# Kernel optimization log

Hardware: AMD Instinct MI355X
Metric: run time of the kernel (lower is better)

## Reference

```python
import jax, jax.numpy as jnp
import numpy as np

SR, WINLEN, HOPLEN = 44100.0, 1024.0, 256.0
B, C, T = 32, 384, 512
MAX_DUR = 0.1          # setup caps duration at 0.1s -> max 13 frames/token
MAX_FRAMES = T * 13    # static padded frame length (jit-compatible upper bound)


def setup_inputs() -> dict:
    key = jax.random.key(0)
    k1, k2, k3, k4 = jax.random.split(key, 4)
    x = jax.random.normal(k1, (B, C, T), dtype=jnp.float32)
    # integer-valued note pitches stored as float (module detaches them anyway)
    notepitch = jax.random.randint(k2, (B, T), 0, 80).astype(jnp.float32)
    duration = jax.random.uniform(k3, (B, T), dtype=jnp.float32) * MAX_DUR
    x_lengths = jax.random.randint(k4, (B,), 1, T + 1)
    return {"x": x, "notepitch": notepitch, "duration": duration, "x_lengths": x_lengths}


def _repeat_counts(duration):
    # expand_size rule from the module:
    #   sr*d - winlen > 0 -> max((sr*d - winlen)/hoplen, 1)
    #   d == 0            -> 0
    #   else              -> 1
    # then int() truncation, clamped at 0.
    fr = SR * duration
    r = jnp.where(fr - WINLEN > 0.0,
                  jnp.maximum((fr - WINLEN) / HOPLEN, 1.0),
                  jnp.where(duration == 0.0, 0.0, 1.0))
    return r.astype(jnp.int32)  # trunc toward zero (values are >= 0)


def reference(x, notepitch, duration, x_lengths):
    r = _repeat_counts(duration)                 # [B, T]
    cum = jnp.cumsum(r, axis=1)                  # [B, T]
    frame_lengths = cum[:, -1]                   # [B]
    pos = jnp.arange(MAX_FRAMES)                 # [F]
    # token index producing each output frame: repeat-interleave via searchsorted
    tok = jax.vmap(lambda c: jnp.searchsorted(c, pos, side="right"))(cum)  # [B, F]
    tok = jnp.minimum(tok, x.shape[-1] - 1)
    mask = pos[None, :] < frame_lengths[:, None]  # [B, F]
    xt = jnp.transpose(x, (0, 2, 1))              # [B, T, C]
    expanded = jnp.take_along_axis(xt, tok[:, :, None], axis=1)  # [B, F, C]
    out = jnp.where(mask[:, :, None], expanded, 0.0)
    out = jnp.transpose(out, (0, 2, 1))           # [B, C, F]
    pitch = jnp.take_along_axis(notepitch, tok, axis=1)
    # module round-trips pitch through LongTensor -> truncation to int
    pitch = jnp.where(mask, pitch.astype(jnp.int32).astype(jnp.float32), 0.0)
    return out, pitch, frame_lengths.astype(jnp.int32)
```

## Files before the change

kernel.cpp:

```cpp
#include <hip/hip_runtime.h>

#define BB 32
#define CC 384
#define TT 512
#define MAXF 6656
#define CG 8
#define NCHUNK 7

typedef float f32x4 __attribute__((ext_vector_type(4)));

__device__ __forceinline__ void nt_store4(float* p, float a, float b, float c, float d) {
    f32x4 v; v.x = a; v.y = b; v.z = c; v.w = d;
    __builtin_nontemporal_store(v, (f32x4*)p);
}

__device__ __forceinline__ void nt_zero4(float* p) {
    f32x4 v = (f32x4)0.0f;
    __builtin_nontemporal_store(v, (f32x4*)p);
}

__device__ __forceinline__ int rep_count(float d) {
    float fr = 44100.0f * d;
    float rf;
    if (fr - 1024.0f > 0.0f) rf = fmaxf((fr - 1024.0f) * (1.0f / 256.0f), 1.0f);
    else rf = (d == 0.0f) ? 0.0f : 1.0f;
    return (int)rf;
}

__global__ __launch_bounds__(256) void lr_fused_co_kernel(
        const float* __restrict__ x,
        const float* __restrict__ notepitch,
        const float* __restrict__ duration,
        float* __restrict__ out,
        float* __restrict__ pitch_out,
        float* __restrict__ fl_out) {
    __shared__ float xs[CG * TT];
    __shared__ float snp[TT];
    __shared__ __attribute__((aligned(16))) unsigned short stok[MAXF];
    __shared__ int wsum[4];

    const int b    = blockIdx.y;
    const int cg   = blockIdx.x;
    const int tid  = threadIdx.x;
    const int lane = tid & 63;
    const int wid  = tid >> 6;
    const bool do_pitch = (cg == 0);

    const float2 dp = *(const float2*)(duration + b * TT + 2 * tid);

    const float4* xsrc = (const float4*)(x + ((size_t)(b * CC + cg * CG)) * TT);
    const float4 xa0 = xsrc[tid];
    const float4 xa1 = xsrc[256 + tid];
    const float4 xa2 = xsrc[512 + tid];
    const float4 xa3 = xsrc[768 + tid];
    float2 np2 = make_float2(0.f, 0.f);
    if (do_pitch) np2 = *(const float2*)(notepitch + b * TT + 2 * tid);

    const int r0 = rep_count(dp.x);
    const int r1 = rep_count(dp.y);
    const int s  = r0 + r1;

    int v = s;
    #pragma unroll
    for (int off = 1; off < 64; off <<= 1) {
        const int t = __shfl_up(v, off, 64);
        if (lane >= off) v += t;
    }
    if (lane == 63) wsum[wid] = v;
    __syncthreads();

    int prefix = 0, total = 0;
    #pragma unroll
    for (int w = 0; w < 4; ++w) {
        const int t = wsum[w];
        total += t;
        if (w < wid) prefix += t;
    }
    const int incl = v + prefix;
    const int excl = incl - s;
    const int fl   = total;

    if (do_pitch && tid == 0) fl_out[b] = (float)fl;

    float* const obase = out + ((size_t)(b * CC + cg * CG)) * MAXF;
    float* const pb    = pitch_out + (size_t)b * MAXF;

    #pragma unroll
    for (int c = 0; c < CG; ++c) {
        float* const ob = obase + (size_t)c * MAXF;
        #pragma unroll
        for (int ch = 0; ch < NCHUNK; ++ch) {
            const int base = ch * 1024;
            const int p0 = base + tid * 4;
            if (base >= fl && p0 < MAXF)
                nt_zero4(ob + p0);
        }
    }
    if (do_pitch) {
        #pragma unroll
        for (int ch = 0; ch < NCHUNK; ++ch) {
            const int base = ch * 1024;
            const int p0 = base + tid * 4;
            if (base >= fl && p0 < MAXF)
                nt_zero4(pb + p0);
        }
    }

    {
        float4* xdst = (float4*)xs;
        xdst[tid] = xa0; xdst[256 + tid] = xa1;
        xdst[512 + tid] = xa2; xdst[768 + tid] = xa3;
    }
    if (do_pitch) *(float2*)(snp + 2 * tid) = np2;

    for (int f = excl; f < excl + r0; ++f)       stok[f] = (unsigned short)(2 * tid);
    for (int f = excl + r0; f < incl; ++f)       stok[f] = (unsigned short)(2 * tid + 1);
    __syncthreads();

    ushort4 tkv[NCHUNK];
    #pragma unroll
    for (int ch = 0; ch < NCHUNK; ++ch) {
        const int p0 = ch * 1024 + tid * 4;
        if (p0 < MAXF) tkv[ch] = *(const ushort4*)(stok + p0);
        else           tkv[ch] = make_ushort4(0, 0, 0, 0);
    }

    #pragma unroll
    for (int c = 0; c < CG; ++c) {
        const float* const xr = xs + c * TT;
        float* const ob = obase + (size_t)c * MAXF;
        #pragma unroll
        for (int ch = 0; ch < NCHUNK; ++ch) {
            const int base = ch * 1024;
            const int p0 = base + tid * 4;
            if (base >= fl || p0 >= MAXF) continue;

            const ushort4 tk = tkv[ch];
            if (base + 1024 <= fl) {
                nt_store4(ob + p0, xr[tk.x], xr[tk.y], xr[tk.z], xr[tk.w]);
            } else {
                const int u0 = min((int)tk.x, TT - 1), u1 = min((int)tk.y, TT - 1);
                const int u2 = min((int)tk.z, TT - 1), u3 = min((int)tk.w, TT - 1);
                const bool m0 = p0 < fl, m1 = p0 + 1 < fl;
                const bool m2 = p0 + 2 < fl, m3 = p0 + 3 < fl;
                nt_store4(ob + p0,
                          m0 ? xr[u0] : 0.f,
                          m1 ? xr[u1] : 0.f,
                          m2 ? xr[u2] : 0.f,
                          m3 ? xr[u3] : 0.f);
            }
        }
    }
    if (do_pitch) {
        #pragma unroll
        for (int ch = 0; ch < NCHUNK; ++ch) {
            const int base = ch * 1024;
            const int p0 = base + tid * 4;
            if (base >= fl || p0 >= MAXF) continue;

            const ushort4 tk = tkv[ch];
            if (base + 1024 <= fl) {
                nt_store4(pb + p0,
                          (float)(int)snp[tk.x], (float)(int)snp[tk.y],
                          (float)(int)snp[tk.z], (float)(int)snp[tk.w]);
            } else {
                const int u0 = min((int)tk.x, TT - 1), u1 = min((int)tk.y, TT - 1);
                const int u2 = min((int)tk.z, TT - 1), u3 = min((int)tk.w, TT - 1);
                const bool m0 = p0 < fl, m1 = p0 + 1 < fl;
                const bool m2 = p0 + 2 < fl, m3 = p0 + 3 < fl;
                nt_store4(pb + p0,
                          m0 ? (float)(int)snp[u0] : 0.f,
                          m1 ? (float)(int)snp[u1] : 0.f,
                          m2 ? (float)(int)snp[u2] : 0.f,
                          m3 ? (float)(int)snp[u3] : 0.f);
            }
        }
    }
}

extern "C" void kernel_launch(void* const* d_in, const int* in_sizes, int n_in,
                              void* d_out, int out_size, void* d_ws, size_t ws_size,
                              hipStream_t stream) {
    (void)in_sizes; (void)n_in; (void)out_size; (void)d_ws; (void)ws_size;

    const float* x         = (const float*)d_in[0];
    const float* notepitch = (const float*)d_in[1];
    const float* duration  = (const float*)d_in[2];

    float* out       = (float*)d_out;
    float* pitch_out = out + (size_t)BB * CC * MAXF;
    float* fl_out    = pitch_out + (size_t)BB * MAXF;

    dim3 g(CC / CG, BB);
    lr_fused_co_kernel<<<g, 256, 0, stream>>>(x, notepitch, duration,
                                              out, pitch_out, fl_out);
}
```

Baseline: 70.48 us.

## Make kernel persistent over channel tiles with register-prefetched x loads

Replaces the 48x32 grid with 256 blocks, each handling six consecutive 8-channel tiles of one batch row. The prefix-scan and token map are built once per block and reused across tiles, and the next tile's x slice is prefetched into registers while the current tile is being written. This amortizes the scan and setup over more output and overlaps loads with stores. In exchange there are fewer blocks (256 on a 256-CU part) and therefore less parallelism for latency hiding, plus extra barriers per tile.

Measured after the change: 70.26 us. Within noise of the previous version (-0.3%).

```diff
diff --git a/kernel.cpp b/kernel.cpp
--- a/kernel.cpp
+++ b/kernel.cpp
@@ -6,6 +6,7 @@
 #define MAXF 6656
 #define CG 8
 #define NCHUNK 7
+#define NTILE 6
 
 typedef float f32x4 __attribute__((ext_vector_type(4)));
 
@@ -27,7 +28,7 @@
     return (int)rf;
 }
 
-__global__ __launch_bounds__(256) void lr_fused_co_kernel(
+__global__ __launch_bounds__(256) void lr_persist_kernel(
         const float* __restrict__ x,
         const float* __restrict__ notepitch,
         const float* __restrict__ duration,
@@ -39,22 +40,23 @@
     __shared__ __attribute__((aligned(16))) unsigned short stok[MAXF];
     __shared__ int wsum[4];
 
-    const int b    = blockIdx.y;
-    const int cg   = blockIdx.x;
+    const int blk  = blockIdx.x;
+    const int b    = blk >> 3;
+    const int cg0  = (blk & 7) * NTILE;
     const int tid  = threadIdx.x;
     const int lane = tid & 63;
     const int wid  = tid >> 6;
-    const bool do_pitch = (cg == 0);
+    const bool pw  = ((blk & 7) == 0);
 
     const float2 dp = *(const float2*)(duration + b * TT + 2 * tid);
 
-    const float4* xsrc = (const float4*)(x + ((size_t)(b * CC + cg * CG)) * TT);
-    const float4 xa0 = xsrc[tid];
-    const float4 xa1 = xsrc[256 + tid];
-    const float4 xa2 = xsrc[512 + tid];
-    const float4 xa3 = xsrc[768 + tid];
+    const float4* xsrc0 = (const float4*)(x + ((size_t)(b * CC + cg0 * CG)) * TT);
+    float4 xa0 = xsrc0[tid];
+    float4 xa1 = xsrc0[256 + tid];
+    float4 xa2 = xsrc0[512 + tid];
+    float4 xa3 = xsrc0[768 + tid];
     float2 np2 = make_float2(0.f, 0.f);
-    if (do_pitch) np2 = *(const float2*)(notepitch + b * TT + 2 * tid);
+    if (pw) np2 = *(const float2*)(notepitch + b * TT + 2 * tid);
 
     const int r0 = rep_count(dp.x);
     const int r1 = rep_count(dp.y);
@@ -80,14 +82,12 @@
     const int excl = incl - s;
     const int fl   = total;
 
-    if (do_pitch && tid == 0) fl_out[b] = (float)fl;
-
-    float* const obase = out + ((size_t)(b * CC + cg * CG)) * MAXF;
+    if (pw && tid == 0) fl_out[b] = (float)fl;
+
+    float* const orow0 = out + ((size_t)(b * CC + cg0 * CG)) * MAXF;
     float* const pb    = pitch_out + (size_t)b * MAXF;
-
-    #pragma unroll
-    for (int c = 0; c < CG; ++c) {
-        float* const ob = obase + (size_t)c * MAXF;
+    for (int c = 0; c < CG * NTILE; ++c) {
+        float* const ob = orow0 + (size_t)c * MAXF;
         #pragma unroll
         for (int ch = 0; ch < NCHUNK; ++ch) {
             const int base = ch * 1024;
@@ -96,7 +96,7 @@
                 nt_zero4(ob + p0);
         }
     }
-    if (do_pitch) {
+    if (pw) {
         #pragma unroll
         for (int ch = 0; ch < NCHUNK; ++ch) {
             const int base = ch * 1024;
@@ -106,15 +106,9 @@
         }
     }
 
-    {
-        float4* xdst = (float4*)xs;
-        xdst[tid] = xa0; xdst[256 + tid] = xa1;
-        xdst[512 + tid] = xa2; xdst[768 + tid] = xa3;
-    }
-    if (do_pitch) *(float2*)(snp + 2 * tid) = np2;
-
     for (int f = excl; f < excl + r0; ++f)       stok[f] = (unsigned short)(2 * tid);
     for (int f = excl + r0; f < incl; ++f)       stok[f] = (unsigned short)(2 * tid + 1);
+    if (pw) *(float2*)(snp + 2 * tid) = np2;
     __syncthreads();
 
     ushort4 tkv[NCHUNK];
@@ -125,56 +119,73 @@
         else           tkv[ch] = make_ushort4(0, 0, 0, 0);
     }
 
-    #pragma unroll
-    for (int c = 0; c < CG; ++c) {
-        const float* const xr = xs + c * TT;
-        float* const ob = obase + (size_t)c * MAXF;
+    for (int t = 0; t < NTILE; ++t) {
+        {
+            float4* xdst = (float4*)xs;
+            xdst[tid] = xa0; xdst[256 + tid] = xa1;
+            xdst[512 + tid] = xa2; xdst[768 + tid] = xa3;
+        }
+        if (t + 1 < NTILE) {
+            const float4* xn =
+                (const float4*)(x + ((size_t)(b * CC + (cg0 + t + 1) * CG)) * TT);
+            xa0 = xn[tid]; xa1 = xn[256 + tid];
+            xa2 = xn[512 + tid]; xa3 = xn[768 + tid];
+        }
+        __syncthreads();
+
+        float* const obase = out + ((size_t)(b * CC + (cg0 + t) * CG)) * MAXF;
         #pragma unroll
-        for (int ch = 0; ch < NCHUNK; ++ch) {
-            const int base = ch * 1024;
-            const int p0 = base + tid * 4;
-            if (base >= fl || p0 >= MAXF) continue;
-
-            const ushort4 tk = tkv[ch];
-            if (base + 1024 <= fl) {
-                nt_store4(ob + p0, xr[tk.x], xr[tk.y], xr[tk.z], xr[tk.w]);
-            } else {
-                const int u0 = min((int)tk.x, TT - 1), u1 = min((int)tk.y, TT - 1);
-                const int u2 = min((int)tk.z, TT - 1), u3 = min((int)tk.w, TT - 1);
-                const bool m0 = p0 < fl, m1 = p0 + 1 < fl;
-                const bool m2 = p0 + 2 < fl, m3 = p0 + 3 < fl;
-                nt_store4(ob + p0,
-                          m0 ? xr[u0] : 0.f,
-                          m1 ? xr[u1] : 0.f,
-                          m2 ? xr[u2] : 0.f,
-                          m3 ? xr[u3] : 0.f);
+        for (int c = 0; c < CG; ++c) {
+            const float* const xr = xs + c * TT;
+            float* const ob = obase + (size_t)c * MAXF;
+            #pragma unroll
+            for (int ch = 0; ch < NCHUNK; ++ch) {
+                const int base = ch * 1024;
+                const int p0 = base + tid * 4;
+                if (base >= fl || p0 >= MAXF) continue;
+
+                const ushort4 tk = tkv[ch];
+                if (base + 1024 <= fl) {
+                    nt_store4(ob + p0, xr[tk.x], xr[tk.y], xr[tk.z], xr[tk.w]);
+                } else {
+                    const int u0 = min((int)tk.x, TT - 1), u1 = min((int)tk.y, TT - 1);
+                    const int u2 = min((int)tk.z, TT - 1), u3 = min((int)tk.w, TT - 1);
+                    const bool m0 = p0 < fl, m1 = p0 + 1 < fl;
+                    const bool m2 = p0 + 2 < fl, m3 = p0 + 3 < fl;
+                    nt_store4(ob + p0,
+                              m0 ? xr[u0] : 0.f,
+                              m1 ? xr[u1] : 0.f,
+                              m2 ? xr[u2] : 0.f,
+                              m3 ? xr[u3] : 0.f);
+                }
             }
         }
-    }
-    if (do_pitch) {
-        #pragma unroll
-        for (int ch = 0; ch < NCHUNK; ++ch) {
-            const int base = ch * 1024;
-            const int p0 = base + tid * 4;
-            if (base >= fl || p0 >= MAXF) continue;
-
-            const ushort4 tk = tkv[ch];
-            if (base + 1024 <= fl) {
-                nt_store4(pb + p0,
-                          (float)(int)snp[tk.x], (float)(int)snp[tk.y],
-                          (float)(int)snp[tk.z], (float)(int)snp[tk.w]);
-            } else {
-                const int u0 = min((int)tk.x, TT - 1), u1 = min((int)tk.y, TT - 1);
-                const int u2 = min((int)tk.z, TT - 1), u3 = min((int)tk.w, TT - 1);
-                const bool m0 = p0 < fl, m1 = p0 + 1 < fl;
-                const bool m2 = p0 + 2 < fl, m3 = p0 + 3 < fl;
-                nt_store4(pb + p0,
-                          m0 ? (float)(int)snp[u0] : 0.f,
-                          m1 ? (float)(int)snp[u1] : 0.f,
-                          m2 ? (float)(int)snp[u2] : 0.f,
-                          m3 ? (float)(int)snp[u3] : 0.f);
+        if (pw && t == 0) {
+            #pragma unroll
+            for (int ch = 0; ch < NCHUNK; ++ch) {
+                const int base = ch * 1024;
+                const int p0 = base + tid * 4;
+                if (base >= fl || p0 >= MAXF) continue;
+
+                const ushort4 tk = tkv[ch];
+                if (base + 1024 <= fl) {
+                    nt_store4(pb + p0,
+                              (float)(int)snp[tk.x], (float)(int)snp[tk.y],
+                              (float)(int)snp[tk.z], (float)(int)snp[tk.w]);
+                } else {
+                    const int u0 = min((int)tk.x, TT - 1), u1 = min((int)tk.y, TT - 1);
+                    const int u2 = min((int)tk.z, TT - 1), u3 = min((int)tk.w, TT - 1);
+                    const bool m0 = p0 < fl, m1 = p0 + 1 < fl;
+                    const bool m2 = p0 + 2 < fl, m3 = p0 + 3 < fl;
+                    nt_store4(pb + p0,
+                              m0 ? (float)(int)snp[u0] : 0.f,
+                              m1 ? (float)(int)snp[u1] : 0.f,
+                              m2 ? (float)(int)snp[u2] : 0.f,
+                              m3 ? (float)(int)snp[u3] : 0.f);
+                }
             }
         }
+        if (t + 1 < NTILE) __syncthreads();
     }
 }
 
@@ -191,7 +202,6 @@
     float* pitch_out = out + (size_t)BB * CC * MAXF;
     float* fl_out    = pitch_out + (size_t)BB * MAXF;
 
-    dim3 g(CC / CG, BB);
-    lr_fused_co_kernel<<<g, 256, 0, stream>>>(x, notepitch, duration,
-                                              out, pitch_out, fl_out);
-}
+    lr_persist_kernel<<<256, 256, 0, stream>>>(x, notepitch, duration,
+                                               out, pitch_out, fl_out);
+}
```
